# Optimization experiments

Measured on AMD Instinct MI355X. Metric: run time of the kernel, lower is better.

The kernel has to match this reference:

```python
import jax, jax.numpy as jnp
import numpy as np

B, T, H = 64, 256, 128

def setup_inputs() -> dict:
    key = jax.random.key(0)
    ks = jax.random.split(key, 10)
    s = 1.0 / np.sqrt(H)
    return {
        "x": jax.random.normal(ks[0], (B, T, 2), jnp.float32),
        "enc_output": jax.random.normal(ks[1], (B, T, H), jnp.float32),
        "h0": jax.random.normal(ks[2], (B, H), jnp.float32) * s,
        "c0": jax.random.normal(ks[3], (B, H), jnp.float32) * s,
        "W1": jax.random.normal(ks[4], (H, H), jnp.float32) * s,
        "W2": jax.random.normal(ks[5], (H, H), jnp.float32) * s,
        "V": jax.random.normal(ks[6], (H,), jnp.float32) * s,
        "Wk": jax.random.normal(ks[7], (2, 4 * H), jnp.float32) * (1.0 / np.sqrt(2.0)),
        "Wr": jax.random.normal(ks[8], (H, 4 * H), jnp.float32) * s,
        "b": jnp.zeros((4 * H,), jnp.float32),
    }


def reference(x, enc_output, h0, c0, W1, W2, V, Wk, Wr, b):
    Bb, Tt, _ = x.shape
    # Precompute W1 @ enc_output once (original recomputes it T times inside K.rnn)
    enc_proj = jnp.einsum('bth,hk->btk', enc_output, W1)  # [B,T,H]

    def lstm_cell(inp, h, c):
        # Keras LSTMCell, gate order i,f,c,o; sigmoid recurrent activation, tanh activation
        z = inp @ Wk + h @ Wr + b  # [B,4H]
        zi, zf, zg, zo = jnp.split(z, 4, axis=-1)
        i = jax.nn.sigmoid(zi)
        f = jax.nn.sigmoid(zf)
        g = jnp.tanh(zg)
        o = jax.nn.sigmoid(zo)
        c_new = f * c + i * g
        h_new = o * jnp.tanh(c_new)
        return h_new, c_new

    def step(carry, _):
        h, c, ptr = carry
        h, c = lstm_cell(ptr, h, c)
        # additive attention over all encoder steps, batched (replaces inner K.rnn)
        scores = jnp.einsum('btk,k->bt', jnp.tanh(enc_proj + (h @ W2)[:, None, :]), V)
        probs = jax.nn.softmax(scores, axis=1)  # [B,T]
        # get_pointer with rank=0: top-1 of descending argsort == argmax
        idx = jnp.argmax(probs, axis=1)  # [B]
        ptr = jnp.take_along_axis(x, idx[:, None, None], axis=1)[:, 0, :]  # [B,2]
        return (h, c, ptr), probs

    ptr0 = jnp.ones((Bb, 2), x.dtype)
    _, probs_seq = jax.lax.scan(step, (h0, c0, ptr0), None, length=Tt)  # [T,B,T]
    return jnp.transpose(probs_seq, (1, 0, 2))  # [B,T,T]
```

## Files before the change

kernel.cpp:

```cpp
#include <hip/hip_runtime.h>
#include <cstddef>

#define TT 256
#define HH 128
#define EST 132
#define SCPS 260

typedef float f2 __attribute__((ext_vector_type(2)));
__device__ __forceinline__ f2 mkf2(float a, float b) { f2 r; r.x = a; r.y = b; return r; }
__device__ __forceinline__ f2 pkfma(f2 a, f2 b, f2 c) { return __builtin_elementwise_fma(a, b, c); }

__device__ __forceinline__ float rdlane(float v, int l) {
  return __int_as_float(__builtin_amdgcn_readlane(__float_as_int(v), l));
}
template<int CTRL>
__device__ __forceinline__ float dpp_mv(float x) {
  return __int_as_float(
      __builtin_amdgcn_mov_dpp(__float_as_int(x), CTRL, 0xF, 0xF, true));
}
__device__ __forceinline__ float wave_max64(float x) {
  x = fmaxf(x, dpp_mv<0xB1>(x));
  x = fmaxf(x, dpp_mv<0x4E>(x));
  x = fmaxf(x, dpp_mv<0x124>(x));
  x = fmaxf(x, dpp_mv<0x128>(x));
  x = fmaxf(x, __shfl_xor(x, 16));
  x = fmaxf(x, __shfl_xor(x, 32));
  return x;
}
__device__ __forceinline__ float wave_sum64(float x) {
  x += dpp_mv<0xB1>(x);
  x += dpp_mv<0x4E>(x);
  x += dpp_mv<0x124>(x);
  x += dpp_mv<0x128>(x);
  x += __shfl_xor(x, 16);
  x += __shfl_xor(x, 32);
  return x;
}
__device__ __forceinline__ float fast_sigmoid(float x) {
  const float L2E = 1.4426950408889634f;
  float y = __builtin_amdgcn_exp2f(-x * L2E);
  return __builtin_amdgcn_rcpf(1.0f + y);
}
__device__ __forceinline__ float fast_tanh(float x) {
  const float C2 = 2.8853900817779268f;
  float y = __builtin_amdgcn_exp2f(x * C2);
  return 1.0f - 2.0f * __builtin_amdgcn_rcpf(1.0f + y);
}

__global__ __attribute__((amdgpu_flat_work_group_size(512, 512),
                          amdgpu_waves_per_eu(2, 2)))
void decoder_kernel(const float* __restrict__ x,
                    const float* __restrict__ enc_output,
                    const float* __restrict__ h0,
                    const float* __restrict__ c0,
                    const float* __restrict__ W1,
                    const float* __restrict__ W2,
                    const float* __restrict__ V,
                    const float* __restrict__ Wk,
                    const float* __restrict__ Wr,
                    const float* __restrict__ bias,
                    float* __restrict__ out)
{
  __shared__ float E[TT * EST];
  __shared__ float zpart[4 * 512];
  __shared__ float scp[8 * SCPS];
  __shared__ float hbuf[HH];
  __shared__ float xlds[2 * TT];

  const int u    = threadIdx.x;
  const int b    = blockIdx.x;
  const int lane = u & 63;
  const int w    = u >> 6;
  const float C2  = 2.8853900817779268f;
  const float L2E = 1.4426950408889634f;
  const f2 one2 = {1.0f, 1.0f};

  {
    const float* encb = enc_output + (size_t)b * TT * HH;
    const int tsub = u >> 4;
    const int ks   = (u & 15) * 8;
    for (int p = 0; p < 8; ++p) {
      const int tt = p * 32 + tsub;
      f2 a0l = {0.f, 0.f}, a0h = {0.f, 0.f};
      f2 a1l = {0.f, 0.f}, a1h = {0.f, 0.f};
      const float4* er4 = (const float4*)(encb + tt * HH);
      for (int j4 = 0; j4 < 32; ++j4) {
        const float4 ev = er4[j4];
        const float* w1p = W1 + (j4 * 4) * HH + ks;
        float4 wa, wb;
        f2 s;
        wa = *(const float4*)(w1p + 0 * HH); wb = *(const float4*)(w1p + 0 * HH + 4);
        s = mkf2(ev.x, ev.x);
        a0l = pkfma(s, mkf2(wa.x, wa.y), a0l); a0h = pkfma(s, mkf2(wa.z, wa.w), a0h);
        a1l = pkfma(s, mkf2(wb.x, wb.y), a1l); a1h = pkfma(s, mkf2(wb.z, wb.w), a1h);
        wa = *(const float4*)(w1p + 1 * HH); wb = *(const float4*)(w1p + 1 * HH + 4);
        s = mkf2(ev.y, ev.y);
        a0l = pkfma(s, mkf2(wa.x, wa.y), a0l); a0h = pkfma(s, mkf2(wa.z, wa.w), a0h);
        a1l = pkfma(s, mkf2(wb.x, wb.y), a1l); a1h = pkfma(s, mkf2(wb.z, wb.w), a1h);
        wa = *(const float4*)(w1p + 2 * HH); wb = *(const float4*)(w1p + 2 * HH + 4);
        s = mkf2(ev.z, ev.z);
        a0l = pkfma(s, mkf2(wa.x, wa.y), a0l); a0h = pkfma(s, mkf2(wa.z, wa.w), a0h);
        a1l = pkfma(s, mkf2(wb.x, wb.y), a1l); a1h = pkfma(s, mkf2(wb.z, wb.w), a1h);
        wa = *(const float4*)(w1p + 3 * HH); wb = *(const float4*)(w1p + 3 * HH + 4);
        s = mkf2(ev.w, ev.w);
        a0l = pkfma(s, mkf2(wa.x, wa.y), a0l); a0h = pkfma(s, mkf2(wa.z, wa.w), a0h);
        a1l = pkfma(s, mkf2(wb.x, wb.y), a1l); a1h = pkfma(s, mkf2(wb.z, wb.w), a1h);
      }
      float4 o0 = {a0l.x, a0l.y, a0h.x, a0h.y};
      float4 o1 = {a1l.x, a1l.y, a1h.x, a1h.y};
      *(float4*)(&E[tt * EST + ks])     = o0;
      *(float4*)(&E[tt * EST + ks + 4]) = o1;
    }
    xlds[u] = x[b * (TT * 2) + u];
  }

  const int kq = u >> 7;
  const int cs = u & 127;
  float4 wr4[32];
  #pragma unroll
  for (int i = 0; i < 32; ++i)
    wr4[i] = *(const float4*)(Wr + (32 * kq + i) * 512 + 4 * cs);
  const int m = 32 * (w & 3) + (lane & 31);
  float wkA[4], wkB[4], bbg[4];
  #pragma unroll
  for (int gg = 0; gg < 4; ++gg) {
    wkA[gg] = Wk[gg * HH + m];
    wkB[gg] = Wk[512 + gg * HH + m];
    bbg[gg] = bias[gg * HH + m];
  }
  float c = c0[b * HH + m];
  const int kk = lane & 15;
  const int jq = lane >> 4;
  f2 w2f2[16];
  #pragma unroll
  for (int i = 0; i < 16; ++i)
    w2f2[i] = mkf2(W2[(32 * jq + 2 * i) * HH + 16 * w + kk],
                   W2[(32 * jq + 2 * i + 1) * HH + 16 * w + kk]);
  const float v2r = -2.0f * V[16 * w + kk];
  float vL[16];
  #pragma unroll
  for (int i = 0; i < 16; ++i) vL[i] = rdlane(v2r, i);
  float ptr0 = 1.0f, ptr1 = 1.0f;
  float svr;
  {
    float v = V[lane] + V[64 + lane];
    svr = wave_sum64(v);
  }

  __syncthreads();

  {
    float* Er = &E[(u >> 1) * EST + 64 * (u & 1)];
    #pragma unroll
    for (int i = 0; i < 16; ++i) {
      float4 ev = *(const float4*)(Er + 4 * i);
      ev.x = __builtin_amdgcn_exp2f(ev.x * C2);
      ev.y = __builtin_amdgcn_exp2f(ev.y * C2);
      ev.z = __builtin_amdgcn_exp2f(ev.z * C2);
      ev.w = __builtin_amdgcn_exp2f(ev.w * C2);
      *(float4*)(Er + 4 * i) = ev;
    }
  }
  {
    float hA0 = h0[(size_t)b * HH + 32 * kq + (lane & 31)];
    f2 zacl = {0.f, 0.f}, zach = {0.f, 0.f};
    #pragma unroll
    for (int i = 0; i < 32; ++i) {
      float hi = rdlane(hA0, i);
      f2 h2 = mkf2(hi, hi);
      zacl = pkfma(h2, mkf2(wr4[i].x, wr4[i].y), zacl);
      zach = pkfma(h2, mkf2(wr4[i].z, wr4[i].w), zach);
    }
    float4 zo = {zacl.x, zacl.y, zach.x, zach.y};
    *(float4*)(&zpart[kq * 512 + 4 * cs]) = zo;
  }
  __syncthreads();

  float* outb = out + (size_t)b * TT * TT;

  #pragma unroll 1
  for (int step = 0; step < TT; ++step) {
    float zpv[16];
    const bool gate_lane = ((lane & 32) == 0 && w < 4);
    if (gate_lane) {
      #pragma unroll
      for (int q = 0; q < 4; ++q) {
        zpv[4 * q + 0] = zpart[q * 512 + 0 * HH + m];
        zpv[4 * q + 1] = zpart[q * 512 + 1 * HH + m];
        zpv[4 * q + 2] = zpart[q * 512 + 2 * HH + m];
        zpv[4 * q + 3] = zpart[q * 512 + 3 * HH + m];
      }
    }
    if (step > 0) {
      if (w < 4) {
        float4 sc = {0.f, 0.f, 0.f, 0.f};
        #pragma unroll
        for (int q = 0; q < 8; ++q) {
          float4 v = *(const float4*)(&scp[q * SCPS + 4 * lane]);
          sc.x += v.x; sc.y += v.y; sc.z += v.z; sc.w += v.w;
        }
        float m4 = fmaxf(fmaxf(sc.x, sc.y), fmaxf(sc.z, sc.w));
        int ttl = (sc.x == m4) ? 0 : (sc.y == m4) ? 1 : (sc.z == m4) ? 2 : 3;
        float mx = wave_max64(m4);
        unsigned long long bal = __ballot(m4 == mx);
        int ls  = __ffsll(bal) - 1;
        int tc  = 4 * lane + ttl;
        int tts = __builtin_amdgcn_readlane(tc, ls);
        const float2 pp = *(const float2*)(&xlds[2 * tts]);
        ptr0 = pp.x;
        ptr1 = pp.y;
      } else {
        float4 sc = {0.f, 0.f, 0.f, 0.f};
        #pragma unroll
        for (int q = 0; q < 8; ++q) {
          float4 v = *(const float4*)(&scp[q * SCPS + 4 * lane]);
          sc.x += v.x; sc.y += v.y; sc.z += v.z; sc.w += v.w;
        }
        sc.x += svr; sc.y += svr; sc.z += svr; sc.w += svr;
        float p0 = __builtin_amdgcn_exp2f((sc.x - 12.0f) * L2E);
        float p1 = __builtin_amdgcn_exp2f((sc.y - 12.0f) * L2E);
        float p2 = __builtin_amdgcn_exp2f((sc.z - 12.0f) * L2E);
        float p3 = __builtin_amdgcn_exp2f((sc.w - 12.0f) * L2E);
        float ws4 = wave_sum64((p0 + p1) + (p2 + p3));
        if ((lane >> 4) == (w - 4)) {
          float rs = __builtin_amdgcn_rcpf(ws4);
          float4 po = {p0 * rs, p1 * rs, p2 * rs, p3 * rs};
          *(float4*)(&outb[(size_t)(step - 1) * TT + 4 * lane]) = po;
        }
      }
    }
    if (gate_lane) {
      float z0 = bbg[0] + ptr0 * wkA[0] + ptr1 * wkB[0];
      float z1 = bbg[1] + ptr0 * wkA[1] + ptr1 * wkB[1];
      float z2 = bbg[2] + ptr0 * wkA[2] + ptr1 * wkB[2];
      float z3 = bbg[3] + ptr0 * wkA[3] + ptr1 * wkB[3];
      z0 += (zpv[0] + zpv[4]) + (zpv[ 8] + zpv[12]);
      z1 += (zpv[1] + zpv[5]) + (zpv[ 9] + zpv[13]);
      z2 += (zpv[2] + zpv[6]) + (zpv[10] + zpv[14]);
      z3 += (zpv[3] + zpv[7]) + (zpv[11] + zpv[15]);
      float ig = fast_sigmoid(z0);
      float fg = fast_sigmoid(z1);
      float gg = fast_tanh(z2);
      float og = fast_sigmoid(z3);
      c = fg * c + ig * gg;
      hbuf[m] = og * fast_tanh(c);
    }
    __syncthreads();

    float Uk;
    {
      f2 cpv = {0.f, 0.f};
      const float4* h4 = (const float4*)(hbuf + 32 * jq);
      #pragma unroll
      for (int i4 = 0; i4 < 8; ++i4) {
        float4 hv = h4[i4];
        cpv = pkfma(mkf2(hv.x, hv.y), w2f2[2 * i4],     cpv);
        cpv = pkfma(mkf2(hv.z, hv.w), w2f2[2 * i4 + 1], cpv);
      }
      float csum = cpv.x + cpv.y;
      csum += __shfl_xor(csum, 16);
      csum += __shfl_xor(csum, 32);
      Uk = __builtin_amdgcn_exp2f(csum * C2);
    }
    {
      const float4* h4 = (const float4*)(hbuf + 32 * kq);
      f2 zacl = {0.f, 0.f}, zach = {0.f, 0.f};
      #pragma unroll
      for (int i4 = 0; i4 < 8; ++i4) {
        float4 hv = h4[i4];
        f2 hx = mkf2(hv.x, hv.x), hy = mkf2(hv.y, hv.y);
        f2 hz = mkf2(hv.z, hv.z), hw = mkf2(hv.w, hv.w);
        zacl = pkfma(hx, mkf2(wr4[4 * i4 + 0].x, wr4[4 * i4 + 0].y), zacl);
        zach = pkfma(hx, mkf2(wr4[4 * i4 + 0].z, wr4[4 * i4 + 0].w), zach);
        zacl = pkfma(hy, mkf2(wr4[4 * i4 + 1].x, wr4[4 * i4 + 1].y), zacl);
        zach = pkfma(hy, mkf2(wr4[4 * i4 + 1].z, wr4[4 * i4 + 1].w), zach);
        zacl = pkfma(hz, mkf2(wr4[4 * i4 + 2].x, wr4[4 * i4 + 2].y), zacl);
        zach = pkfma(hz, mkf2(wr4[4 * i4 + 2].z, wr4[4 * i4 + 2].w), zach);
        zacl = pkfma(hw, mkf2(wr4[4 * i4 + 3].x, wr4[4 * i4 + 3].y), zacl);
        zach = pkfma(hw, mkf2(wr4[4 * i4 + 3].z, wr4[4 * i4 + 3].w), zach);
      }
      float4 zo = {zacl.x, zacl.y, zach.x, zach.y};
      *(float4*)(&zpart[kq * 512 + 4 * cs]) = zo;
    }
    {
      float uL[16];
      #pragma unroll
      for (int i = 0; i < 16; ++i) uL[i] = rdlane(Uk, i);
      f2 uf2[8];
      #pragma unroll
      for (int j = 0; j < 8; ++j) uf2[j] = mkf2(uL[2 * j], uL[2 * j + 1]);
      #pragma unroll
      for (int tt = 0; tt < 4; ++tt) {
        const float* Er = &E[(64 * tt + lane) * EST + 16 * w];
        float4 e0 = *(const float4*)(Er + 0);
        float4 e1 = *(const float4*)(Er + 4);
        float4 e2 = *(const float4*)(Er + 8);
        float4 e3 = *(const float4*)(Er + 12);
        float a0 = 0.0f, a1 = 0.0f;
        f2 tp;
        float n;
        tp = pkfma(mkf2(e0.x, e0.y), uf2[0], one2);
        n  = fmaf(vL[ 1], tp.x, vL[ 0] * tp.y);
        a0 = fmaf(n, __builtin_amdgcn_rcpf(tp.x * tp.y), a0);
        tp = pkfma(mkf2(e0.z, e0.w), uf2[1], one2);
        n  = fmaf(vL[ 3], tp.x, vL[ 2] * tp.y);
        a1 = fmaf(n, __builtin_amdgcn_rcpf(tp.x * tp.y), a1);
        tp = pkfma(mkf2(e1.x, e1.y), uf2[2], one2);
        n  = fmaf(vL[ 5], tp.x, vL[ 4] * tp.y);
        a0 = fmaf(n, __builtin_amdgcn_rcpf(tp.x * tp.y), a0);
        tp = pkfma(mkf2(e1.z, e1.w), uf2[3], one2);
        n  = fmaf(vL[ 7], tp.x, vL[ 6] * tp.y);
        a1 = fmaf(n, __builtin_amdgcn_rcpf(tp.x * tp.y), a1);
        tp = pkfma(mkf2(e2.x, e2.y), uf2[4], one2);
        n  = fmaf(vL[ 9], tp.x, vL[ 8] * tp.y);
        a0 = fmaf(n, __builtin_amdgcn_rcpf(tp.x * tp.y), a0);
        tp = pkfma(mkf2(e2.z, e2.w), uf2[5], one2);
        n  = fmaf(vL[11], tp.x, vL[10] * tp.y);
        a1 = fmaf(n, __builtin_amdgcn_rcpf(tp.x * tp.y), a1);
        tp = pkfma(mkf2(e3.x, e3.y), uf2[6], one2);
        n  = fmaf(vL[13], tp.x, vL[12] * tp.y);
        a0 = fmaf(n, __builtin_amdgcn_rcpf(tp.x * tp.y), a0);
        tp = pkfma(mkf2(e3.z, e3.w), uf2[7], one2);
        n  = fmaf(vL[15], tp.x, vL[14] * tp.y);
        a1 = fmaf(n, __builtin_amdgcn_rcpf(tp.x * tp.y), a1);
        scp[w * SCPS + 64 * tt + lane] = a0 + a1;
      }
    }
    __syncthreads();
  }

  if (w >= 4) {
    float4 sc = {0.f, 0.f, 0.f, 0.f};
    #pragma unroll
    for (int q = 0; q < 8; ++q) {
      float4 v = *(const float4*)(&scp[q * SCPS + 4 * lane]);
      sc.x += v.x; sc.y += v.y; sc.z += v.z; sc.w += v.w;
    }
    sc.x += svr; sc.y += svr; sc.z += svr; sc.w += svr;
    float p0 = __builtin_amdgcn_exp2f((sc.x - 12.0f) * L2E);
    float p1 = __builtin_amdgcn_exp2f((sc.y - 12.0f) * L2E);
    float p2 = __builtin_amdgcn_exp2f((sc.z - 12.0f) * L2E);
    float p3 = __builtin_amdgcn_exp2f((sc.w - 12.0f) * L2E);
    float ws4 = wave_sum64((p0 + p1) + (p2 + p3));
    if ((lane >> 4) == (w - 4)) {
      float rs = __builtin_amdgcn_rcpf(ws4);
      float4 po = {p0 * rs, p1 * rs, p2 * rs, p3 * rs};
      *(float4*)(&outb[(size_t)255 * TT + 4 * lane]) = po;
    }
  }
}

extern "C" void kernel_launch(void* const* d_in, const int* in_sizes, int n_in,
                              void* d_out, int out_size, void* d_ws, size_t ws_size,
                              hipStream_t stream) {
  (void)in_sizes; (void)n_in; (void)d_ws; (void)ws_size; (void)out_size;
  const float* x    = (const float*)d_in[0];
  const float* enc  = (const float*)d_in[1];
  const float* h0   = (const float*)d_in[2];
  const float* c0   = (const float*)d_in[3];
  const float* W1   = (const float*)d_in[4];
  const float* W2   = (const float*)d_in[5];
  const float* V    = (const float*)d_in[6];
  const float* Wk   = (const float*)d_in[7];
  const float* Wr   = (const float*)d_in[8];
  const float* bias = (const float*)d_in[9];
  float* out = (float*)d_out;

  decoder_kernel<<<64, 512, 0, stream>>>(x, enc, h0, c0, W1, W2, V, Wk, Wr, bias, out);
}
```

Measured before the change: 767.4 us.

## Merge tanh-sum fractions to halve reciprocals and keep x pointers in registers

In the attention score loop, pairs of rational tanh terms are combined over a common denominator, so there is one reciprocal per four hidden units instead of per two. The x coordinates move out of LDS into per-lane registers and are picked with readlane after the argmax, and the W2 dot product is split into two accumulators for more ILP. The merged denominator is a product of four (1+e*U) factors, which may overflow or lose precision for large values.

Result: no change. 775.8 us (+1.1%).

```diff
diff --git a/kernel.cpp b/kernel.cpp
--- a/kernel.cpp
+++ b/kernel.cpp
@@ -65,7 +65,6 @@
   __shared__ float zpart[4 * 512];
   __shared__ float scp[8 * SCPS];
   __shared__ float hbuf[HH];
-  __shared__ float xlds[2 * TT];
 
   const int u    = threadIdx.x;
   const int b    = blockIdx.x;
@@ -111,7 +110,6 @@
       *(float4*)(&E[tt * EST + ks])     = o0;
       *(float4*)(&E[tt * EST + ks + 4]) = o1;
     }
-    xlds[u] = x[b * (TT * 2) + u];
   }
 
   const int kq = u >> 7;
@@ -129,6 +127,10 @@
     bbg[gg] = bias[gg * HH + m];
   }
   float c = c0[b * HH + m];
+  float2 xr0 = *(const float2*)(x + b * (TT * 2) + 2 * (0 * 64 + lane));
+  float2 xr1 = *(const float2*)(x + b * (TT * 2) + 2 * (1 * 64 + lane));
+  float2 xr2 = *(const float2*)(x + b * (TT * 2) + 2 * (2 * 64 + lane));
+  float2 xr3 = *(const float2*)(x + b * (TT * 2) + 2 * (3 * 64 + lane));
   const int kk = lane & 15;
   const int jq = lane >> 4;
   f2 w2f2[16];
@@ -206,9 +208,11 @@
         int ls  = __ffsll(bal) - 1;
         int tc  = 4 * lane + ttl;
         int tts = __builtin_amdgcn_readlane(tc, ls);
-        const float2 pp = *(const float2*)(&xlds[2 * tts]);
-        ptr0 = pp.x;
-        ptr1 = pp.y;
+        int j   = tts >> 6;
+        int ll  = tts & 63;
+        float2 cand = (j == 0) ? xr0 : (j == 1) ? xr1 : (j == 2) ? xr2 : xr3;
+        ptr0 = rdlane(cand.x, ll);
+        ptr1 = rdlane(cand.y, ll);
       } else {
         float4 sc = {0.f, 0.f, 0.f, 0.f};
         #pragma unroll
@@ -249,14 +253,15 @@
 
     float Uk;
     {
-      f2 cpv = {0.f, 0.f};
+      f2 cpa = {0.f, 0.f}, cpb = {0.f, 0.f};
       const float4* h4 = (const float4*)(hbuf + 32 * jq);
       #pragma unroll
       for (int i4 = 0; i4 < 8; ++i4) {
         float4 hv = h4[i4];
-        cpv = pkfma(mkf2(hv.x, hv.y), w2f2[2 * i4],     cpv);
-        cpv = pkfma(mkf2(hv.z, hv.w), w2f2[2 * i4 + 1], cpv);
-      }
+        cpa = pkfma(mkf2(hv.x, hv.y), w2f2[2 * i4],     cpa);
+        cpb = pkfma(mkf2(hv.z, hv.w), w2f2[2 * i4 + 1], cpb);
+      }
+      f2 cpv = cpa + cpb;
       float csum = cpv.x + cpv.y;
       csum += __shfl_xor(csum, 16);
       csum += __shfl_xor(csum, 32);
@@ -297,32 +302,32 @@
         float4 e2 = *(const float4*)(Er + 8);
         float4 e3 = *(const float4*)(Er + 12);
         float a0 = 0.0f, a1 = 0.0f;
-        f2 tp;
-        float n;
-        tp = pkfma(mkf2(e0.x, e0.y), uf2[0], one2);
-        n  = fmaf(vL[ 1], tp.x, vL[ 0] * tp.y);
-        a0 = fmaf(n, __builtin_amdgcn_rcpf(tp.x * tp.y), a0);
-        tp = pkfma(mkf2(e0.z, e0.w), uf2[1], one2);
-        n  = fmaf(vL[ 3], tp.x, vL[ 2] * tp.y);
-        a1 = fmaf(n, __builtin_amdgcn_rcpf(tp.x * tp.y), a1);
-        tp = pkfma(mkf2(e1.x, e1.y), uf2[2], one2);
-        n  = fmaf(vL[ 5], tp.x, vL[ 4] * tp.y);
-        a0 = fmaf(n, __builtin_amdgcn_rcpf(tp.x * tp.y), a0);
-        tp = pkfma(mkf2(e1.z, e1.w), uf2[3], one2);
-        n  = fmaf(vL[ 7], tp.x, vL[ 6] * tp.y);
-        a1 = fmaf(n, __builtin_amdgcn_rcpf(tp.x * tp.y), a1);
-        tp = pkfma(mkf2(e2.x, e2.y), uf2[4], one2);
-        n  = fmaf(vL[ 9], tp.x, vL[ 8] * tp.y);
-        a0 = fmaf(n, __builtin_amdgcn_rcpf(tp.x * tp.y), a0);
-        tp = pkfma(mkf2(e2.z, e2.w), uf2[5], one2);
-        n  = fmaf(vL[11], tp.x, vL[10] * tp.y);
-        a1 = fmaf(n, __builtin_amdgcn_rcpf(tp.x * tp.y), a1);
-        tp = pkfma(mkf2(e3.x, e3.y), uf2[6], one2);
-        n  = fmaf(vL[13], tp.x, vL[12] * tp.y);
-        a0 = fmaf(n, __builtin_amdgcn_rcpf(tp.x * tp.y), a0);
-        tp = pkfma(mkf2(e3.z, e3.w), uf2[7], one2);
-        n  = fmaf(vL[15], tp.x, vL[14] * tp.y);
-        a1 = fmaf(n, __builtin_amdgcn_rcpf(tp.x * tp.y), a1);
+        f2 tA, tB;
+        float nA, dA, nB, dB, N, Dn;
+        tA = pkfma(mkf2(e0.x, e0.y), uf2[0], one2);
+        tB = pkfma(mkf2(e0.z, e0.w), uf2[1], one2);
+        nA = fmaf(vL[ 1], tA.x, vL[ 0] * tA.y);  dA = tA.x * tA.y;
+        nB = fmaf(vL[ 3], tB.x, vL[ 2] * tB.y);  dB = tB.x * tB.y;
+        N  = fmaf(nA, dB, nB * dA);              Dn = dA * dB;
+        a0 = fmaf(N, __builtin_amdgcn_rcpf(Dn), a0);
+        tA = pkfma(mkf2(e1.x, e1.y), uf2[2], one2);
+        tB = pkfma(mkf2(e1.z, e1.w), uf2[3], one2);
+        nA = fmaf(vL[ 5], tA.x, vL[ 4] * tA.y);  dA = tA.x * tA.y;
+        nB = fmaf(vL[ 7], tB.x, vL[ 6] * tB.y);  dB = tB.x * tB.y;
+        N  = fmaf(nA, dB, nB * dA);              Dn = dA * dB;
+        a1 = fmaf(N, __builtin_amdgcn_rcpf(Dn), a1);
+        tA = pkfma(mkf2(e2.x, e2.y), uf2[4], one2);
+        tB = pkfma(mkf2(e2.z, e2.w), uf2[5], one2);
+        nA = fmaf(vL[ 9], tA.x, vL[ 8] * tA.y);  dA = tA.x * tA.y;
+        nB = fmaf(vL[11], tB.x, vL[10] * tB.y);  dB = tB.x * tB.y;
+        N  = fmaf(nA, dB, nB * dA);              Dn = dA * dB;
+        a0 = fmaf(N, __builtin_amdgcn_rcpf(Dn), a0);
+        tA = pkfma(mkf2(e3.x, e3.y), uf2[6], one2);
+        tB = pkfma(mkf2(e3.z, e3.w), uf2[7], one2);
+        nA = fmaf(vL[13], tA.x, vL[12] * tA.y);  dA = tA.x * tA.y;
+        nB = fmaf(vL[15], tB.x, vL[14] * tB.y);  dB = tB.x * tB.y;
+        N  = fmaf(nA, dB, nB * dA);              Dn = dA * dB;
+        a1 = fmaf(N, __builtin_amdgcn_rcpf(Dn), a1);
         scp[w * SCPS + 64 * tt + lane] = a0 + a1;
       }
     }
```
